# Kernel optimization log

Measured on AMD Instinct MI355X. Metric: run time of the kernel, lower is better.

The kernel has to match this reference:

```python
import jax, jax.numpy as jnp
import numpy as np

HEAD = 10
HEAD_DIM = 50
B, LQ, LK = 8, 2048, 1024
Q_IN, K_IN, PROJ = 1124, 10100, 500


def setup_inputs() -> dict:
    key = jax.random.key(0)
    ks = jax.random.split(key, 10)
    inp = {
        "query": jax.random.normal(ks[0], (B, LQ, Q_IN), dtype=jnp.float32),
        "key": jax.random.normal(ks[1], (B, LK, K_IN), dtype=jnp.float32),
        "value": jax.random.normal(ks[2], (B, LK), dtype=jnp.float32),
        # params (torch Linear: y = x W^T + b; store W already transposed)
        "Wq": jax.random.normal(ks[3], (Q_IN, PROJ), dtype=jnp.float32) * (1.0 / np.sqrt(Q_IN)),
        "bq": jnp.zeros((PROJ,), dtype=jnp.float32),
        "Wk": jax.random.normal(ks[4], (K_IN, PROJ), dtype=jnp.float32) * (1.0 / np.sqrt(K_IN)),
        "bk": jnp.zeros((PROJ,), dtype=jnp.float32),
        "W1": jax.random.normal(ks[5], (HEAD, 10), dtype=jnp.float32) * (1.0 / np.sqrt(HEAD)),
        "b1": jnp.zeros((10,), dtype=jnp.float32),
        "W2": jax.random.normal(ks[6], (10, 1), dtype=jnp.float32) * (1.0 / np.sqrt(10)),
        "b2": jnp.zeros((1,), dtype=jnp.float32),
    }
    return inp


def reference(query, key, value, Wq, bq, Wk, bk, W1, b1, W2, b2):
    # projections -> [B, L, head, head_dim]
    q = (query @ Wq + bq).reshape(B, LQ, HEAD, HEAD_DIM)
    k = (key @ Wk + bk).reshape(B, LK, HEAD, HEAD_DIM)
    # scores [B, head, Lq, Lk], scaled by sqrt(head_dim)
    scores = jnp.einsum("bqhd,bkhd->bhqk", q, k) / np.sqrt(HEAD_DIM).astype(np.float32)
    attn = jax.nn.softmax(scores, axis=-1)
    # value is per-head scalar (value_dim=1, repeated across heads)
    out = jnp.einsum("bhqk,bk->bqh", attn, value)  # [B, Lq, head]
    h = jax.nn.relu(out @ W1 + b1)
    y = jax.nn.relu(h @ W2 + b2)  # [B, Lq, 1]
    return y[..., 0]  # [B, Lq]
```

## Files before the change

### kernel.cpp

```cpp
#include <hip/hip_runtime.h>
#include <math.h>

#define HEADS 10
#define HDIM  50
#define BSZ   8
#define SLQ   2048
#define SLK   1024
#define QIN   1124
#define KIN   10100
#define PROJ  500
#define NPAD  512
#define HPAD  64
#define ROWP  (HEADS * HPAD)

typedef short bf16x8 __attribute__((ext_vector_type(8)));
typedef float f32x4  __attribute__((ext_vector_type(4)));

__device__ __forceinline__ unsigned short bf16_rne(float x) {
    unsigned int u = __float_as_uint(x);
    u += 0x7fffu + ((u >> 16) & 1u);
    return (unsigned short)(u >> 16);
}
__device__ __forceinline__ float bf16_to_f32(unsigned short h) {
    return __uint_as_float(((unsigned int)h) << 16);
}
__device__ __forceinline__ void split_hl(float x, unsigned short& h, unsigned short& l) {
    h = bf16_rne(x);
    l = bf16_rne(x - bf16_to_f32(h));
}

__device__ __forceinline__ void gload_lds16(const void* g, void* l) {
    __builtin_amdgcn_global_load_lds(
        (const __attribute__((address_space(1))) void*)g,
        (__attribute__((address_space(3))) void*)l, 16, 0, 0);
}

__global__ __launch_bounds__(256)
void conv_split_act(const float* __restrict__ A, int r0, int rows, int K, int Kp,
                    short* __restrict__ H, short* __restrict__ L) {
    const int gpr = Kp >> 3;
    const long long idx = (long long)blockIdx.x * 256 + threadIdx.x;
    if (idx >= (long long)rows * gpr) return;
    const int r = (int)(idx / gpr);
    const int g = (int)(idx % gpr);
    const int k0 = g << 3;
    const float* src = A + (size_t)(r0 + r) * K;
    float x[8];
    if (k0 + 8 <= K) {
        const float4 v0 = *(const float4*)(src + k0);
        const float4 v1 = *(const float4*)(src + k0 + 4);
        x[0]=v0.x; x[1]=v0.y; x[2]=v0.z; x[3]=v0.w;
        x[4]=v1.x; x[5]=v1.y; x[6]=v1.z; x[7]=v1.w;
    } else {
        #pragma unroll
        for (int j = 0; j < 8; j++) x[j] = (k0 + j < K) ? src[k0 + j] : 0.f;
    }
    unsigned short h[8], l[8];
    #pragma unroll
    for (int j = 0; j < 8; j++) split_hl(x[j], h[j], l[j]);
    *(bf16x8*)(H + (size_t)r * Kp + k0) = *(bf16x8*)h;
    *(bf16x8*)(L + (size_t)r * Kp + k0) = *(bf16x8*)l;
}

__global__ __launch_bounds__(256)
void conv_split_wT(const float* __restrict__ W, int K, int N, int Kp,
                   short* __restrict__ H, short* __restrict__ L) {
    const int gpr = Kp >> 3;
    const int idx = blockIdx.x * 256 + threadIdx.x;
    if (idx >= NPAD * gpr) return;
    const int g = idx / NPAD;
    const int n = idx % NPAD;
    const int k0 = g << 3;
    float x[8];
    #pragma unroll
    for (int j = 0; j < 8; j++)
        x[j] = (n < N && k0 + j < K) ? W[(size_t)(k0 + j) * N + n] : 0.f;
    unsigned short h[8], l[8];
    #pragma unroll
    for (int j = 0; j < 8; j++) split_hl(x[j], h[j], l[j]);
    *(bf16x8*)(H + (size_t)n * Kp + k0) = *(bf16x8*)h;
    *(bf16x8*)(L + (size_t)n * Kp + k0) = *(bf16x8*)l;
}

__global__ __launch_bounds__(256)
void zero_pads(short* __restrict__ H, short* __restrict__ L, int rows) {
    const int idx = blockIdx.x * 256 + threadIdx.x;
    const int tot = rows * HEADS * (HPAD - HDIM);
    if (idx >= tot) return;
    const int d = HDIM + idx % (HPAD - HDIM);
    const int t = idx / (HPAD - HDIM);
    const int hh = t % HEADS;
    const int row = t / HEADS;
    const size_t off = (size_t)row * ROWP + hh * HPAD + d;
    H[off] = 0; L[off] = 0;
}

__global__ __launch_bounds__(256)
void gemm_split(const short* __restrict__ Ah, const short* __restrict__ Al,
                const short* __restrict__ BTh, const short* __restrict__ BTl,
                const float* __restrict__ bias,
                short* __restrict__ Ch, short* __restrict__ Cl, int Kp) {
    __shared__ short sAh[128 * 32];
    __shared__ short sAl[128 * 32];
    __shared__ short sBh[64 * 32];
    __shared__ short sBl[64 * 32];

    const int tid = threadIdx.x;
    const int lane = tid & 63;
    const int wid = tid >> 6;
    const int m0 = blockIdx.x * 128;
    const int n0 = blockIdx.y * 64;
    const int wm = (wid >> 1) * 64;
    const int wn = (wid & 1) * 32;

    f32x4 acc[4][2];
    #pragma unroll
    for (int i = 0; i < 4; i++)
        #pragma unroll
        for (int j = 0; j < 2; j++) acc[i][j] = (f32x4)(0.f);

    const int sr = lane >> 2;
    const int sg = (lane & 3) ^ ((lane >> 3) & 3);
    const int kg = lane >> 4;
    const int fr = lane & 15;

    int aoff[4], boff[2];
    #pragma unroll
    for (int i = 0; i < 4; i++) {
        const int r = wm + i * 16 + fr;
        aoff[i] = r * 32 + ((kg ^ ((r >> 1) & 3)) << 3);
    }
    #pragma unroll
    for (int j = 0; j < 2; j++) {
        const int r = wn + j * 16 + fr;
        boff[j] = r * 32 + ((kg ^ ((r >> 1) & 3)) << 3);
    }

    for (int k0 = 0; k0 < Kp; k0 += 32) {
        __syncthreads();
        #pragma unroll
        for (int t = 0; t < 2; t++) {
            const int is = wid + t * 4;
            const size_t grow = (size_t)(m0 + is * 16 + sr) * Kp + k0 + sg * 8;
            gload_lds16(Ah + grow, &sAh[is * 512]);
            gload_lds16(Al + grow, &sAl[is * 512]);
        }
        {
            const size_t grow = (size_t)(n0 + wid * 16 + sr) * Kp + k0 + sg * 8;
            gload_lds16(BTh + grow, &sBh[wid * 512]);
            gload_lds16(BTl + grow, &sBl[wid * 512]);
        }
        __syncthreads();

        bf16x8 ah[4], al[4], bh[2], bl[2];
        #pragma unroll
        for (int i = 0; i < 4; i++) {
            ah[i] = *(const bf16x8*)&sAh[aoff[i]];
            al[i] = *(const bf16x8*)&sAl[aoff[i]];
        }
        #pragma unroll
        for (int j = 0; j < 2; j++) {
            bh[j] = *(const bf16x8*)&sBh[boff[j]];
            bl[j] = *(const bf16x8*)&sBl[boff[j]];
        }
        #pragma unroll
        for (int i = 0; i < 4; i++) {
            #pragma unroll
            for (int j = 0; j < 2; j++) {
                acc[i][j] = __builtin_amdgcn_mfma_f32_16x16x32_bf16(ah[i], bh[j], acc[i][j], 0, 0, 0);
                acc[i][j] = __builtin_amdgcn_mfma_f32_16x16x32_bf16(al[i], bh[j], acc[i][j], 0, 0, 0);
                acc[i][j] = __builtin_amdgcn_mfma_f32_16x16x32_bf16(ah[i], bl[j], acc[i][j], 0, 0, 0);
            }
        }
    }

    #pragma unroll
    for (int i = 0; i < 4; i++) {
        #pragma unroll
        for (int j = 0; j < 2; j++) {
            const int n = n0 + wn + j * 16 + (lane & 15);
            if (n < PROJ) {
                const unsigned hh = (unsigned)n / 50u;
                const unsigned dd = (unsigned)n % 50u;
                const float bv = bias[n];
                #pragma unroll
                for (int r = 0; r < 4; r++) {
                    const int m = m0 + wm + i * 16 + (lane >> 4) * 4 + r;
                    const float val = acc[i][j][r] + bv;
                    unsigned short vh, vl;
                    split_hl(val, vh, vl);
                    const size_t off = (size_t)m * ROWP + hh * HPAD + dd;
                    Ch[off] = vh;
                    Cl[off] = vl;
                }
            }
        }
    }
}

__global__ __launch_bounds__(256)
void attn_mfma(const short* __restrict__ qH, const short* __restrict__ qL,
               const short* __restrict__ kH, const short* __restrict__ kL,
               const float* __restrict__ value, float* __restrict__ out) {
    const int bid = blockIdx.x;
    const int qt = bid & 63;
    const int h  = (bid >> 6) % HEADS;
    const int b  = bid / (64 * HEADS);
    const int q0 = qt * 32;

    const int tid = threadIdx.x;
    const int lane = tid & 63;
    const int w = tid >> 6;
    const int col = lane & 15;
    const int quad = lane >> 4;

    bf16x8 qh[2][2], ql[2][2];
    #pragma unroll
    for (int rs = 0; rs < 2; rs++) {
        #pragma unroll
        for (int t = 0; t < 2; t++) {
            const size_t off = (size_t)((size_t)b * SLQ + q0 + rs * 16 + col) * ROWP
                               + h * HPAD + t * 32 + quad * 8;
            qh[rs][t] = *(const bf16x8*)(qH + off);
            ql[rs][t] = *(const bf16x8*)(qL + off);
        }
    }

    float m_[2][4], l_[2][4], o_[2][4];
    #pragma unroll
    for (int rs = 0; rs < 2; rs++)
        #pragma unroll
        for (int r = 0; r < 4; r++) { m_[rs][r] = -1e30f; l_[rs][r] = 0.f; o_[rs][r] = 0.f; }

    const float scale = 0.14142135623730950f;

    for (int it = 0; it < 4; it++) {
        const int k0 = w * 256 + it * 64;

        f32x4 acc[2][4];
        #pragma unroll
        for (int rs = 0; rs < 2; rs++)
            #pragma unroll
            for (int cs = 0; cs < 4; cs++) acc[rs][cs] = (f32x4)(0.f);

        #pragma unroll
        for (int t = 0; t < 2; t++) {
            bf16x8 kh[4], kl[4];
            #pragma unroll
            for (int cs = 0; cs < 4; cs++) {
                const size_t off = (size_t)((size_t)b * SLK + k0 + cs * 16 + col) * ROWP
                                   + h * HPAD + t * 32 + quad * 8;
                kh[cs] = *(const bf16x8*)(kH + off);
                kl[cs] = *(const bf16x8*)(kL + off);
            }
            #pragma unroll
            for (int cs = 0; cs < 4; cs++) {
                #pragma unroll
                for (int rs = 0; rs < 2; rs++) {
                    acc[rs][cs] = __builtin_amdgcn_mfma_f32_16x16x32_bf16(qh[rs][t], kh[cs], acc[rs][cs], 0, 0, 0);
                    acc[rs][cs] = __builtin_amdgcn_mfma_f32_16x16x32_bf16(ql[rs][t], kh[cs], acc[rs][cs], 0, 0, 0);
                    acc[rs][cs] = __builtin_amdgcn_mfma_f32_16x16x32_bf16(qh[rs][t], kl[cs], acc[rs][cs], 0, 0, 0);
                }
            }
        }

        float v4[4];
        #pragma unroll
        for (int cs = 0; cs < 4; cs++)
            v4[cs] = value[(size_t)b * SLK + k0 + cs * 16 + col];

        #pragma unroll
        for (int rs = 0; rs < 2; rs++) {
            #pragma unroll
            for (int r = 0; r < 4; r++) {
                float mt = acc[rs][0][r];
                mt = fmaxf(mt, acc[rs][1][r]);
                mt = fmaxf(mt, acc[rs][2][r]);
                mt = fmaxf(mt, acc[rs][3][r]);
                #pragma unroll
                for (int off = 1; off < 16; off <<= 1)
                    mt = fmaxf(mt, __shfl_xor(mt, off));
                const float mn = fmaxf(m_[rs][r], mt);
                const float alpha = __expf((m_[rs][r] - mn) * scale);
                float pl = 0.f, po = 0.f;
                #pragma unroll
                for (int cs = 0; cs < 4; cs++) {
                    const float p = __expf((acc[rs][cs][r] - mn) * scale);
                    pl += p;
                    po += p * v4[cs];
                }
                l_[rs][r] = l_[rs][r] * alpha + pl;
                o_[rs][r] = o_[rs][r] * alpha + po;
                m_[rs][r] = mn;
            }
        }
    }

    #pragma unroll
    for (int rs = 0; rs < 2; rs++) {
        #pragma unroll
        for (int r = 0; r < 4; r++) {
            #pragma unroll
            for (int off = 1; off < 16; off <<= 1) {
                l_[rs][r] += __shfl_xor(l_[rs][r], off);
                o_[rs][r] += __shfl_xor(o_[rs][r], off);
            }
        }
    }

    __shared__ float sm[4][32], sl[4][32], so[4][32];
    if (col == 0) {
        #pragma unroll
        for (int rs = 0; rs < 2; rs++)
            #pragma unroll
            for (int r = 0; r < 4; r++) {
                const int row = rs * 16 + quad * 4 + r;
                sm[w][row] = m_[rs][r];
                sl[w][row] = l_[rs][r];
                so[w][row] = o_[rs][r];
            }
    }
    __syncthreads();

    if (tid < 32) {
        const int row = tid;
        float M = sm[0][row];
        #pragma unroll
        for (int ww = 1; ww < 4; ww++) M = fmaxf(M, sm[ww][row]);
        float L = 0.f, O = 0.f;
        #pragma unroll
        for (int ww = 0; ww < 4; ww++) {
            const float e = __expf((sm[ww][row] - M) * scale);
            L += sl[ww][row] * e;
            O += so[ww][row] * e;
        }
        out[((size_t)b * SLQ + q0 + row) * HEADS + h] = O / L;
    }
}

__global__ __launch_bounds__(256)
void sgemm_bias(const float* __restrict__ A, const float* __restrict__ B,
                const float* __restrict__ bias, float* __restrict__ C,
                int M, int N, int K, int ldc) {
    __shared__ __align__(16) float As[16][68];
    __shared__ __align__(16) float Bs[16][64];
    const int tid = threadIdx.x;
    const int tx = tid & 15, ty = tid >> 4;
    const int m0 = blockIdx.y * 64, n0 = blockIdx.x * 64;
    const int arow = tid >> 2, ak4 = (tid & 3) * 4;
    const int bk = tid >> 4, bc4 = (tid & 15) * 4;

    float acc[4][4];
    #pragma unroll
    for (int i = 0; i < 4; i++)
        #pragma unroll
        for (int j = 0; j < 4; j++) acc[i][j] = 0.f;

    for (int k0 = 0; k0 < K; k0 += 16) {
        float4 av;
        if (k0 + 16 <= K) {
            av = *(const float4*)(A + (size_t)(m0 + arow) * K + k0 + ak4);
        } else {
            float t[4] = {0.f, 0.f, 0.f, 0.f};
            const float* Ar = A + (size_t)(m0 + arow) * K;
            #pragma unroll
            for (int j = 0; j < 4; j++) if (k0 + ak4 + j < K) t[j] = Ar[k0 + ak4 + j];
            av = make_float4(t[0], t[1], t[2], t[3]);
        }
        As[ak4 + 0][arow] = av.x; As[ak4 + 1][arow] = av.y;
        As[ak4 + 2][arow] = av.z; As[ak4 + 3][arow] = av.w;

        float4 bv = make_float4(0.f, 0.f, 0.f, 0.f);
        const int gk = k0 + bk;
        if (gk < K) {
            if (n0 + bc4 + 3 < N) bv = *(const float4*)(B + (size_t)gk * N + n0 + bc4);
            else {
                const float* Br = B + (size_t)gk * N;
                float t[4] = {0.f, 0.f, 0.f, 0.f};
                #pragma unroll
                for (int j = 0; j < 4; j++) if (n0 + bc4 + j < N) t[j] = Br[n0 + bc4 + j];
                bv = make_float4(t[0], t[1], t[2], t[3]);
            }
        }
        *(float4*)&Bs[bk][bc4] = bv;
        __syncthreads();
        #pragma unroll
        for (int kk = 0; kk < 16; kk++) {
            const float4 a = *(const float4*)&As[kk][ty * 4];
            const float4 b = *(const float4*)&Bs[kk][tx * 4];
            const float ar[4] = {a.x, a.y, a.z, a.w};
            const float br[4] = {b.x, b.y, b.z, b.w};
            #pragma unroll
            for (int i = 0; i < 4; i++)
                #pragma unroll
                for (int j = 0; j < 4; j++) acc[i][j] += ar[i] * br[j];
        }
        __syncthreads();
    }
    #pragma unroll
    for (int i = 0; i < 4; i++) {
        const int m = m0 + ty * 4 + i;
        #pragma unroll
        for (int j = 0; j < 4; j++) {
            const int n = n0 + tx * 4 + j;
            if (n < N) C[(size_t)m * ldc + n] = acc[i][j] + bias[n];
        }
    }
}

__global__ __launch_bounds__(256)
void attn_fused(const float* __restrict__ q, const float* __restrict__ k,
                const float* __restrict__ value, float* __restrict__ out, int ldp) {
    const int bid = blockIdx.x;
    const int qt = bid & 31;
    const int h  = (bid >> 5) % HEADS;
    const int b  = bid / (32 * HEADS);
    const int q0 = qt * 64;

    __shared__ __align__(16) float Qs[HDIM][68];
    __shared__ __align__(16) float Ks[HDIM][68];
    __shared__ float Vs[64];

    const int tid = threadIdx.x;
    const int tx = tid & 15, ty = tid >> 4;

    for (int idx = tid; idx < 64 * HDIM; idx += 256) {
        const int r = idx / HDIM, d = idx % HDIM;
        Qs[d][r] = q[((size_t)b * SLQ + q0 + r) * ldp + h * HDIM + d];
    }

    float m_[4], l_[4], o_[4];
    #pragma unroll
    for (int i = 0; i < 4; i++) { m_[i] = -1e30f; l_[i] = 0.f; o_[i] = 0.f; }
    const float scale = 0.14142135623730950f;

    for (int kt = 0; kt < SLK / 64; kt++) {
        __syncthreads();
        for (int idx = tid; idx < 64 * HDIM; idx += 256) {
            const int r = idx / HDIM, d = idx % HDIM;
            Ks[d][r] = k[((size_t)b * SLK + kt * 64 + r) * ldp + h * HDIM + d];
        }
        if (tid < 64) Vs[tid] = value[(size_t)b * SLK + kt * 64 + tid];
        __syncthreads();

        float s[4][4];
        #pragma unroll
        for (int i = 0; i < 4; i++)
            #pragma unroll
            for (int j = 0; j < 4; j++) s[i][j] = 0.f;

        #pragma unroll
        for (int d = 0; d < HDIM; d++) {
            const float4 a = *(const float4*)&Qs[d][ty * 4];
            const float4 bb = *(const float4*)&Ks[d][tx * 4];
            const float ar[4] = {a.x, a.y, a.z, a.w};
            const float br[4] = {bb.x, bb.y, bb.z, bb.w};
            #pragma unroll
            for (int i = 0; i < 4; i++)
                #pragma unroll
                for (int j = 0; j < 4; j++) s[i][j] += ar[i] * br[j];
        }

        #pragma unroll
        for (int i = 0; i < 4; i++) {
            float tmax = -1e30f;
            #pragma unroll
            for (int j = 0; j < 4; j++) { s[i][j] *= scale; tmax = fmaxf(tmax, s[i][j]); }
            #pragma unroll
            for (int off = 1; off < 16; off <<= 1) tmax = fmaxf(tmax, __shfl_xor(tmax, off));
            const float mnew = fmaxf(m_[i], tmax);
            const float alpha = __expf(m_[i] - mnew);
            float ls = 0.f, lo = 0.f;
            #pragma unroll
            for (int j = 0; j < 4; j++) {
                const float p = __expf(s[i][j] - mnew);
                ls += p;
                lo += p * Vs[tx * 4 + j];
            }
            #pragma unroll
            for (int off = 1; off < 16; off <<= 1) { ls += __shfl_xor(ls, off); lo += __shfl_xor(lo, off); }
            l_[i] = l_[i] * alpha + ls;
            o_[i] = o_[i] * alpha + lo;
            m_[i] = mnew;
        }
    }

    if (tx == 0) {
        #pragma unroll
        for (int i = 0; i < 4; i++) {
            const int r = q0 + ty * 4 + i;
            out[((size_t)b * SLQ + r) * HEADS + h] = o_[i] / l_[i];
        }
    }
}

__global__ __launch_bounds__(256)
void mlp_kernel(const float* __restrict__ attn, const float* __restrict__ W1,
                const float* __restrict__ b1, const float* __restrict__ W2,
                const float* __restrict__ b2, float* __restrict__ y) {
    const int idx = blockIdx.x * blockDim.x + threadIdx.x;
    if (idx >= BSZ * SLQ) return;
    float o[HEADS];
    #pragma unroll
    for (int i = 0; i < HEADS; i++) o[i] = attn[(size_t)idx * HEADS + i];
    float yv = 0.f;
    #pragma unroll
    for (int j = 0; j < 10; j++) {
        float hv = b1[j];
        #pragma unroll
        for (int i = 0; i < HEADS; i++) hv += o[i] * W1[i * 10 + j];
        hv = fmaxf(hv, 0.f);
        yv += hv * W2[j];
    }
    yv += b2[0];
    y[idx] = fmaxf(yv, 0.f);
}

extern "C" void kernel_launch(void* const* d_in, const int* in_sizes, int n_in,
                              void* d_out, int out_size, void* d_ws, size_t ws_size,
                              hipStream_t stream) {
    const float* query = (const float*)d_in[0];
    const float* key   = (const float*)d_in[1];
    const float* value = (const float*)d_in[2];
    const float* Wq    = (const float*)d_in[3];
    const float* bq    = (const float*)d_in[4];
    const float* Wk    = (const float*)d_in[5];
    const float* bk    = (const float*)d_in[6];
    const float* W1    = (const float*)d_in[7];
    const float* b1    = (const float*)d_in[8];
    const float* W2    = (const float*)d_in[9];
    const float* b2    = (const float*)d_in[10];
    float* y = (float*)d_out;

    const int KP_K = 10112;
    const int KP_Q = 1152;
    const int MK = BSZ * SLK, MQ = BSZ * SLQ;
    char* ws = (char*)d_ws;

    size_t off = 0;
    short* kph = (short*)(ws + off); off += (size_t)MK * ROWP * 2;
    short* kpl = (short*)(ws + off); off += (size_t)MK * ROWP * 2;
    short* qph = (short*)(ws + off); off += (size_t)MQ * ROWP * 2;
    short* qpl = (short*)(ws + off); off += (size_t)MQ * ROWP * 2;
    float* aout = (float*)(ws + off); off += (size_t)MQ * HEADS * 4;
    short* wBTh = (short*)(ws + off); off += (size_t)NPAD * KP_K * 2;
    short* wBTl = (short*)(ws + off); off += (size_t)NPAD * KP_K * 2;
    short* Ascr = (short*)(ws + off);
    const size_t avail = (ws_size > off) ? (ws_size - off) : 0;

    long long cmk = (long long)(avail / ((size_t)KP_K * 4)) & ~127LL;
    long long cmq = (long long)(avail / ((size_t)KP_Q * 4)) & ~127LL;
    if (cmk > MK) cmk = MK;
    if (cmq > MQ) cmq = MQ;
    const bool tierA = (cmk >= 128) && (cmq >= 128);

    if (tierA) {
        {
            const int totK = MK * HEADS * (HPAD - HDIM);
            const int totQ = MQ * HEADS * (HPAD - HDIM);
            zero_pads<<<(totK + 255) / 256, 256, 0, stream>>>(kph, kpl, MK);
            zero_pads<<<(totQ + 255) / 256, 256, 0, stream>>>(qph, qpl, MQ);
        }
        conv_split_wT<<<(NPAD * (KP_K / 8) + 255) / 256, 256, 0, stream>>>(
            Wk, KIN, PROJ, KP_K, wBTh, wBTl);
        {
            short* Ah = Ascr;
            short* Al = Ascr + (size_t)cmk * KP_K;
            for (int r0 = 0; r0 < MK; r0 += (int)cmk) {
                const int rows = (MK - r0 < cmk) ? (MK - r0) : (int)cmk;
                const long long ng = (long long)rows * (KP_K / 8);
                conv_split_act<<<(unsigned)((ng + 255) / 256), 256, 0, stream>>>(
                    key, r0, rows, KIN, KP_K, Ah, Al);
                dim3 grid(rows / 128, NPAD / 64);
                gemm_split<<<grid, 256, 0, stream>>>(Ah, Al, wBTh, wBTl, bk,
                                                     kph + (size_t)r0 * ROWP,
                                                     kpl + (size_t)r0 * ROWP, KP_K);
            }
        }
        conv_split_wT<<<(NPAD * (KP_Q / 8) + 255) / 256, 256, 0, stream>>>(
            Wq, QIN, PROJ, KP_Q, wBTh, wBTl);
        {
            short* Ah = Ascr;
            short* Al = Ascr + (size_t)cmq * KP_Q;
            for (int r0 = 0; r0 < MQ; r0 += (int)cmq) {
                const int rows = (MQ - r0 < cmq) ? (MQ - r0) : (int)cmq;
                const long long ng = (long long)rows * (KP_Q / 8);
                conv_split_act<<<(unsigned)((ng + 255) / 256), 256, 0, stream>>>(
                    query, r0, rows, QIN, KP_Q, Ah, Al);
                dim3 grid(rows / 128, NPAD / 64);
                gemm_split<<<grid, 256, 0, stream>>>(Ah, Al, wBTh, wBTl, bq,
                                                     qph + (size_t)r0 * ROWP,
                                                     qpl + (size_t)r0 * ROWP, KP_Q);
            }
        }
        attn_mfma<<<BSZ * HEADS * (SLQ / 32), 256, 0, stream>>>(
            qph, qpl, kph, kpl, value, aout);
        mlp_kernel<<<(MQ + 255) / 256, 256, 0, stream>>>(aout, W1, b1, W2, b2, y);
    } else {
        const size_t fb_pad = ((size_t)MK * NPAD + (size_t)MQ * NPAD + (size_t)MQ * HEADS) * 4;
        const int ldp = (ws_size >= fb_pad) ? NPAD : PROJ;
        float* kp2 = (float*)ws;
        float* qp2 = kp2 + (size_t)MK * ldp;
        float* ao2 = qp2 + (size_t)MQ * ldp;
        {
            dim3 grid((PROJ + 63) / 64, MK / 64);
            sgemm_bias<<<grid, 256, 0, stream>>>(key, Wk, bk, kp2, MK, PROJ, KIN, ldp);
        }
        {
            dim3 grid((PROJ + 63) / 64, MQ / 64);
            sgemm_bias<<<grid, 256, 0, stream>>>(query, Wq, bq, qp2, MQ, PROJ, QIN, ldp);
        }
        attn_fused<<<BSZ * HEADS * (SLQ / 64), 256, 0, stream>>>(qp2, kp2, value, ao2, ldp);
        mlp_kernel<<<(MQ + 255) / 256, 256, 0, stream>>>(ao2, W1, b1, W2, b2, y);
    }
}
```

Measured before the change: 1.247 ms.

## Split-K the key projection GEMM and fold softmax scale into Q

The key projection GEMM (M=8192, K=10112) now runs as a split-K kernel with four K slices writing fp32 partials, followed by a combine kernel that sums the partials, adds bias and emits the hi/lo bf16 padded layout. The original grid has only 64x8 blocks, so the split-K grid is meant to fill more compute units. The 1/sqrt(d) scale is folded into the query projection epilogue, which removes the per-score multiply in attention. The change also narrows index math in the activation conversion kernel to 32-bit. The cost is extra workspace and global traffic for the partials, plus one more kernel launch.

```diff
diff --git a/kernel.cpp b/kernel.cpp
--- a/kernel.cpp
+++ b/kernel.cpp
@@ -12,6 +12,10 @@
 #define NPAD  512
 #define HPAD  64
 #define ROWP  (HEADS * HPAD)
+#define KP_K  10112
+#define KP_Q  1152
+#define KSPLIT 4
+#define KSLICE (KP_K / KSPLIT)
 
 typedef short bf16x8 __attribute__((ext_vector_type(8)));
 typedef float f32x4  __attribute__((ext_vector_type(4)));
@@ -39,10 +43,10 @@
 void conv_split_act(const float* __restrict__ A, int r0, int rows, int K, int Kp,
                     short* __restrict__ H, short* __restrict__ L) {
     const int gpr = Kp >> 3;
-    const long long idx = (long long)blockIdx.x * 256 + threadIdx.x;
-    if (idx >= (long long)rows * gpr) return;
-    const int r = (int)(idx / gpr);
-    const int g = (int)(idx % gpr);
+    const int idx = blockIdx.x * 256 + threadIdx.x;
+    if (idx >= rows * gpr) return;
+    const int r = idx / gpr;
+    const int g = idx - r * gpr;
     const int k0 = g << 3;
     const float* src = A + (size_t)(r0 + r) * K;
     float x[8];
@@ -96,10 +100,130 @@
 }
 
 __global__ __launch_bounds__(256)
+void gemm_splitk(const short* __restrict__ Ah, const short* __restrict__ Al,
+                 const short* __restrict__ BTh, const short* __restrict__ BTl,
+                 float* __restrict__ P, int Mc) {
+    __shared__ short sAh[128 * 32];
+    __shared__ short sAl[128 * 32];
+    __shared__ short sBh[64 * 32];
+    __shared__ short sBl[64 * 32];
+
+    const int tid = threadIdx.x;
+    const int lane = tid & 63;
+    const int wid = tid >> 6;
+    const int m0 = blockIdx.x * 128;
+    const int n0 = blockIdx.y * 64;
+    const int s  = blockIdx.z;
+    const int kbeg = s * KSLICE;
+    const int kend = kbeg + KSLICE;
+    const int wm = (wid >> 1) * 64;
+    const int wn = (wid & 1) * 32;
+
+    f32x4 acc[4][2];
+    #pragma unroll
+    for (int i = 0; i < 4; i++)
+        #pragma unroll
+        for (int j = 0; j < 2; j++) acc[i][j] = (f32x4)(0.f);
+
+    const int sr = lane >> 2;
+    const int sg = (lane & 3) ^ ((lane >> 3) & 3);
+    const int kg = lane >> 4;
+    const int fr = lane & 15;
+
+    int aoff[4], boff[2];
+    #pragma unroll
+    for (int i = 0; i < 4; i++) {
+        const int r = wm + i * 16 + fr;
+        aoff[i] = r * 32 + ((kg ^ ((r >> 1) & 3)) << 3);
+    }
+    #pragma unroll
+    for (int j = 0; j < 2; j++) {
+        const int r = wn + j * 16 + fr;
+        boff[j] = r * 32 + ((kg ^ ((r >> 1) & 3)) << 3);
+    }
+
+    for (int k0 = kbeg; k0 < kend; k0 += 32) {
+        __syncthreads();
+        #pragma unroll
+        for (int t = 0; t < 2; t++) {
+            const int is = wid + t * 4;
+            const size_t grow = (size_t)(m0 + is * 16 + sr) * KP_K + k0 + sg * 8;
+            gload_lds16(Ah + grow, &sAh[is * 512]);
+            gload_lds16(Al + grow, &sAl[is * 512]);
+        }
+        {
+            const size_t grow = (size_t)(n0 + wid * 16 + sr) * KP_K + k0 + sg * 8;
+            gload_lds16(BTh + grow, &sBh[wid * 512]);
+            gload_lds16(BTl + grow, &sBl[wid * 512]);
+        }
+        __syncthreads();
+
+        bf16x8 ah[4], al[4], bh[2], bl[2];
+        #pragma unroll
+        for (int i = 0; i < 4; i++) {
+            ah[i] = *(const bf16x8*)&sAh[aoff[i]];
+            al[i] = *(const bf16x8*)&sAl[aoff[i]];
+        }
+        #pragma unroll
+        for (int j = 0; j < 2; j++) {
+            bh[j] = *(const bf16x8*)&sBh[boff[j]];
+            bl[j] = *(const bf16x8*)&sBl[boff[j]];
+        }
+        #pragma unroll
+        for (int i = 0; i < 4; i++) {
+            #pragma unroll
+            for (int j = 0; j < 2; j++) {
+                acc[i][j] = __builtin_amdgcn_mfma_f32_16x16x32_bf16(ah[i], bh[j], acc[i][j], 0, 0, 0);
+                acc[i][j] = __builtin_amdgcn_mfma_f32_16x16x32_bf16(al[i], bh[j], acc[i][j], 0, 0, 0);
+                acc[i][j] = __builtin_amdgcn_mfma_f32_16x16x32_bf16(ah[i], bl[j], acc[i][j], 0, 0, 0);
+            }
+        }
+    }
+
+    float* Ps = P + (size_t)s * Mc * NPAD;
+    #pragma unroll
+    for (int i = 0; i < 4; i++) {
+        #pragma unroll
+        for (int j = 0; j < 2; j++) {
+            const int n = n0 + wn + j * 16 + (lane & 15);
+            #pragma unroll
+            for (int r = 0; r < 4; r++) {
+                const int m = m0 + wm + i * 16 + (lane >> 4) * 4 + r;
+                Ps[(size_t)m * NPAD + n] = acc[i][j][r];
+            }
+        }
+    }
+}
+
+__global__ __launch_bounds__(256)
+void combine_splitk(const float* __restrict__ P, const float* __restrict__ bias,
+                    short* __restrict__ Ch, short* __restrict__ Cl,
+                    int Mc, float cscale) {
+    const int idx = blockIdx.x * 256 + threadIdx.x;
+    if (idx >= Mc * NPAD) return;
+    const int m = idx >> 9;
+    const int n = idx & (NPAD - 1);
+    if (n >= PROJ) return;
+    float v = 0.f;
+    #pragma unroll
+    for (int s = 0; s < KSPLIT; s++)
+        v += P[(size_t)s * Mc * NPAD + idx];
+    v = (v + bias[n]) * cscale;
+    const unsigned hh = (unsigned)n / 50u;
+    const unsigned dd = (unsigned)n % 50u;
+    unsigned short vh, vl;
+    split_hl(v, vh, vl);
+    const size_t off = (size_t)m * ROWP + hh * HPAD + dd;
+    Ch[off] = vh;
+    Cl[off] = vl;
+}
+
+__global__ __launch_bounds__(256)
 void gemm_split(const short* __restrict__ Ah, const short* __restrict__ Al,
                 const short* __restrict__ BTh, const short* __restrict__ BTl,
                 const float* __restrict__ bias,
-                short* __restrict__ Ch, short* __restrict__ Cl, int Kp) {
+                short* __restrict__ Ch, short* __restrict__ Cl, int Kp,
+                float cscale) {
     __shared__ short sAh[128 * 32];
     __shared__ short sAl[128 * 32];
     __shared__ short sBh[64 * 32];
@@ -186,7 +310,7 @@
                 #pragma unroll
                 for (int r = 0; r < 4; r++) {
                     const int m = m0 + wm + i * 16 + (lane >> 4) * 4 + r;
-                    const float val = acc[i][j][r] + bv;
+                    const float val = (acc[i][j][r] + bv) * cscale;
                     unsigned short vh, vl;
                     split_hl(val, vh, vl);
                     const size_t off = (size_t)m * ROWP + hh * HPAD + dd;
@@ -231,8 +355,6 @@
     for (int rs = 0; rs < 2; rs++)
         #pragma unroll
         for (int r = 0; r < 4; r++) { m_[rs][r] = -1e30f; l_[rs][r] = 0.f; o_[rs][r] = 0.f; }
-
-    const float scale = 0.14142135623730950f;
 
     for (int it = 0; it < 4; it++) {
         const int k0 = w * 256 + it * 64;
@@ -281,11 +403,11 @@
                 for (int off = 1; off < 16; off <<= 1)
                     mt = fmaxf(mt, __shfl_xor(mt, off));
                 const float mn = fmaxf(m_[rs][r], mt);
-                const float alpha = __expf((m_[rs][r] - mn) * scale);
+                const float alpha = __expf(m_[rs][r] - mn);
                 float pl = 0.f, po = 0.f;
                 #pragma unroll
                 for (int cs = 0; cs < 4; cs++) {
-                    const float p = __expf((acc[rs][cs][r] - mn) * scale);
+                    const float p = __expf(acc[rs][cs][r] - mn);
                     pl += p;
                     po += p * v4[cs];
                 }
@@ -330,7 +452,7 @@
         float L = 0.f, O = 0.f;
         #pragma unroll
         for (int ww = 0; ww < 4; ww++) {
-            const float e = __expf((sm[ww][row] - M) * scale);
+            const float e = __expf(sm[ww][row] - M);
             L += sl[ww][row] * e;
             O += so[ww][row] * e;
         }
@@ -532,9 +654,8 @@
     const float* b2    = (const float*)d_in[10];
     float* y = (float*)d_out;
 
-    const int KP_K = 10112;
-    const int KP_Q = 1152;
     const int MK = BSZ * SLK, MQ = BSZ * SLQ;
+    const float qscale = 0.14142135623730950f;
     char* ws = (char*)d_ws;
 
     size_t off = 0;
@@ -545,14 +666,16 @@
     float* aout = (float*)(ws + off); off += (size_t)MQ * HEADS * 4;
     short* wBTh = (short*)(ws + off); off += (size_t)NPAD * KP_K * 2;
     short* wBTl = (short*)(ws + off); off += (size_t)NPAD * KP_K * 2;
-    short* Ascr = (short*)(ws + off);
+    char* scratch = ws + off;
     const size_t avail = (ws_size > off) ? (ws_size - off) : 0;
 
-    long long cmk = (long long)(avail / ((size_t)KP_K * 4)) & ~127LL;
-    long long cmq = (long long)(avail / ((size_t)KP_Q * 4)) & ~127LL;
-    if (cmk > MK) cmk = MK;
-    if (cmq > MQ) cmq = MQ;
-    const bool tierA = (cmk >= 128) && (cmq >= 128);
+    const size_t perK = (size_t)NPAD * KSPLIT * 4 + (size_t)KP_K * 4;
+    long long ck = (long long)(avail / perK) & ~127LL;
+    if (ck > MK) ck = MK;
+    long long cq = (long long)(avail / ((size_t)KP_Q * 4)) & ~127LL;
+    if (cq > MQ) cq = MQ;
+
+    const bool tierA = (ck >= 128) && (cq >= 128);
 
     if (tierA) {
         {
@@ -564,33 +687,36 @@
         conv_split_wT<<<(NPAD * (KP_K / 8) + 255) / 256, 256, 0, stream>>>(
             Wk, KIN, PROJ, KP_K, wBTh, wBTl);
         {
-            short* Ah = Ascr;
-            short* Al = Ascr + (size_t)cmk * KP_K;
-            for (int r0 = 0; r0 < MK; r0 += (int)cmk) {
-                const int rows = (MK - r0 < cmk) ? (MK - r0) : (int)cmk;
-                const long long ng = (long long)rows * (KP_K / 8);
-                conv_split_act<<<(unsigned)((ng + 255) / 256), 256, 0, stream>>>(
+            float* P = (float*)scratch;
+            short* Ah = (short*)(scratch + (size_t)ck * NPAD * KSPLIT * 4);
+            short* Al = Ah + (size_t)ck * KP_K;
+            for (int r0 = 0; r0 < MK; r0 += (int)ck) {
+                const int rows = (MK - r0 < ck) ? (MK - r0) : (int)ck;
+                const int ng = rows * (KP_K / 8);
+                conv_split_act<<<(ng + 255) / 256, 256, 0, stream>>>(
                     key, r0, rows, KIN, KP_K, Ah, Al);
-                dim3 grid(rows / 128, NPAD / 64);
-                gemm_split<<<grid, 256, 0, stream>>>(Ah, Al, wBTh, wBTl, bk,
-                                                     kph + (size_t)r0 * ROWP,
-                                                     kpl + (size_t)r0 * ROWP, KP_K);
+                dim3 grid(rows / 128, NPAD / 64, KSPLIT);
+                gemm_splitk<<<grid, 256, 0, stream>>>(Ah, Al, wBTh, wBTl, P, rows);
+                combine_splitk<<<(rows * NPAD + 255) / 256, 256, 0, stream>>>(
+                    P, bk, kph + (size_t)r0 * ROWP, kpl + (size_t)r0 * ROWP,
+                    rows, 1.0f);
             }
         }
         conv_split_wT<<<(NPAD * (KP_Q / 8) + 255) / 256, 256, 0, stream>>>(
             Wq, QIN, PROJ, KP_Q, wBTh, wBTl);
         {
-            short* Ah = Ascr;
-            short* Al = Ascr + (size_t)cmq * KP_Q;
-            for (int r0 = 0; r0 < MQ; r0 += (int)cmq) {
-                const int rows = (MQ - r0 < cmq) ? (MQ - r0) : (int)cmq;
-                const long long ng = (long long)rows * (KP_Q / 8);
-                conv_split_act<<<(unsigned)((ng + 255) / 256), 256, 0, stream>>>(
+            short* Ah = (short*)scratch;
+            short* Al = Ah + (size_t)cq * KP_Q;
+            for (int r0 = 0; r0 < MQ; r0 += (int)cq) {
+                const int rows = (MQ - r0 < cq) ? (MQ - r0) : (int)cq;
+                const int ng = rows * (KP_Q / 8);
+                conv_split_act<<<(ng + 255) / 256, 256, 0, stream>>>(
                     query, r0, rows, QIN, KP_Q, Ah, Al);
                 dim3 grid(rows / 128, NPAD / 64);
                 gemm_split<<<grid, 256, 0, stream>>>(Ah, Al, wBTh, wBTl, bq,
                                                      qph + (size_t)r0 * ROWP,
-                                                     qpl + (size_t)r0 * ROWP, KP_Q);
+                                                     qpl + (size_t)r0 * ROWP,
+                                                     KP_Q, qscale);
             }
         }
         attn_mfma<<<BSZ * HEADS * (SLQ / 32), 256, 0, stream>>>(
```

Measured after the change: 1.248 ms. No clear change (+0.0%).
